# Performance work log

Measured on AMD Instinct MI355X. Metric: run time of the kernel, lower is better.

The kernel has to match this reference:

```python
import jax, jax.numpy as jnp
import numpy as np

H, Wd, Z = 480, 480, 2
BN_EPS = 1e-3  # PointPillars-style BatchNorm1d(eps=1e-3)


def setup_inputs() -> dict:
    key = jax.random.key(0)
    ks = jax.random.split(key, 5)
    bs, seq, N, Cin, C = 2, 1, 20000, 4, 64
    features = jax.random.normal(ks[0], (bs, seq, N, Cin), dtype=jnp.float32)
    cx = jax.random.randint(ks[1], (bs, seq, N), 0, H)
    cy = jax.random.randint(ks[2], (bs, seq, N), 0, Wd)
    cz = jax.random.randint(ks[3], (bs, seq, N), 0, Z)
    coords = jnp.stack([cx, cy, cz], axis=-1).astype(jnp.int64)
    W = jax.random.normal(ks[4], (C, Cin), dtype=jnp.float32) * 0.1
    gamma = jnp.ones((C,), jnp.float32)
    beta = jnp.zeros((C,), jnp.float32)
    running_mean = jnp.zeros((C,), jnp.float32)
    running_var = jnp.ones((C,), jnp.float32)
    return {"features": features, "coords": coords, "W": W, "gamma": gamma,
            "beta": beta, "running_mean": running_mean, "running_var": running_var}


def reference(features, coords, W, gamma, beta, running_mean, running_var):
    bs, seq, N, Cin = features.shape
    feats = features.reshape(bs * seq, N, Cin)          # [B, N, 4]
    co = coords.reshape(bs * seq, N, 3)
    # flattened voxel index: x*W*Z + y*Z + z, in [0, H*W*Z)
    idx = co[:, :, 0] * (Wd * Z) + co[:, :, 1] * Z + co[:, :, 2]  # [B, N]
    # linear (no bias) + BatchNorm1d (inference stats) + ReLU
    x = jnp.einsum('bnc,uc->bnu', feats, W)             # [B, N, 64]
    x = (x - running_mean) * (gamma / jnp.sqrt(running_var + BN_EPS)) + beta
    x = jax.nn.relu(x)
    B, n, c = x.shape
    # scatter-max into a zero-initialized dense grid (matches torch scatter reduce='max' into zeros)
    x_max = jnp.zeros((B, H * Wd * Z, c), x.dtype)
    x_max = x_max.at[jnp.arange(B)[:, None], idx].max(x)  # [B, HWZ, C]
    # [B, HWZ, C] -> [B, C, H, W, Z] -> [B, Z, C, H, W] -> [B, Z*C, H, W]
    x_max = jnp.transpose(x_max, (0, 2, 1)).reshape(B, c, H, Wd, Z)
    x_max = jnp.transpose(x_max, (0, 4, 1, 2, 3)).reshape(B, Z * c, H, Wd)
    x_perm = jnp.transpose(x, (0, 2, 1))                # [B, C, N]
    return x_perm, jnp.squeeze(x_max)
```

## Files before the change

### kernel.cpp

```cpp
#include <hip/hip_runtime.h>

#define HH  480
#define WW  480
#define ZZ  2
#define CC  64
#define CIN 4
#define BN_EPS 1e-3f
#define ROWS  (2 * ZZ * HH)
#define MAXR  256
#define CHALF 32
#define TPAD  484

__global__ __launch_bounds__(256) void pfn_clear_cnt(int* __restrict__ rowcnt)
{
    int i = blockIdx.x * blockDim.x + threadIdx.x;
    if (i < ROWS) rowcnt[i] = 0;
}

__global__ __launch_bounds__(256) void pfn_pass_a(
    const float* __restrict__ feats,
    const int*   __restrict__ coords,
    const float* __restrict__ W,
    const float* __restrict__ gamma,
    const float* __restrict__ beta,
    const float* __restrict__ rmean,
    const float* __restrict__ rvar,
    float*  __restrict__ out0,
    float4* __restrict__ rowf4,
    int*    __restrict__ roww,
    int*    __restrict__ rowcnt,
    int N, int B)
{
    int gid = blockIdx.x * blockDim.x + threadIdx.x;
    int total = B * N;
    if (gid >= total) return;
    int n = gid % N;
    int b = gid / N;

    float4 f = *reinterpret_cast<const float4*>(feats + (long)gid * CIN);

    #pragma unroll 8
    for (int c = 0; c < CC; ++c) {
        float scale = gamma[c] * rsqrtf(rvar[c] + BN_EPS);
        float bias  = beta[c] - rmean[c] * scale;
        float v = f.x * W[c*4+0] + f.y * W[c*4+1] + f.z * W[c*4+2] + f.w * W[c*4+3];
        v = fmaxf(v * scale + bias, 0.0f);
        out0[((long)(b * CC + c)) * N + n] = v;
    }

    int cx = coords[(long)gid*3 + 0];
    int cy = coords[(long)gid*3 + 1];
    int cz = coords[(long)gid*3 + 2];
    int row = (b * ZZ + cz) * HH + cx;
    int k = atomicAdd(&rowcnt[row], 1);
    if (k < MAXR) {
        rowf4[(long)row * MAXR + k] = f;
        roww [(long)row * MAXR + k] = cy;
    }
}

__global__ __launch_bounds__(512) void pfn_pass_b(
    const float4* __restrict__ rowf4,
    const int*    __restrict__ roww,
    const int*    __restrict__ rowcnt,
    const float*  __restrict__ W,
    const float*  __restrict__ gamma,
    const float*  __restrict__ beta,
    const float*  __restrict__ rmean,
    const float*  __restrict__ rvar,
    float* __restrict__ out1)
{
    int bid  = blockIdx.x;
    int half = bid & 1;
    int row  = bid >> 1;
    int h = row % HH;
    int z = (row / HH) % ZZ;
    int b = row / (HH * ZZ);
    const int c0 = half * CHALF;
    const int tid = threadIdx.x;

    __shared__ float tile[CHALF][TPAD];
    __shared__ float lw[4][CHALF], lsc[CHALF], lbi[CHALF];

    float4* t4 = reinterpret_cast<float4*>(&tile[0][0]);
    const int n4z = CHALF * TPAD / 4;
    for (int i = tid; i < n4z; i += 512)
        t4[i] = make_float4(0.f, 0.f, 0.f, 0.f);
    if (tid < CHALF) {
        int c = c0 + tid;
        float s = gamma[c] * rsqrtf(rvar[c] + BN_EPS);
        lsc[tid] = s;
        lbi[tid] = beta[c] - rmean[c] * s;
        lw[0][tid] = W[c*4+0]; lw[1][tid] = W[c*4+1];
        lw[2][tid] = W[c*4+2]; lw[3][tid] = W[c*4+3];
    }
    __syncthreads();

    int cnt = rowcnt[row];
    cnt = cnt < MAXR ? cnt : MAXR;
    const long rb = (long)row * MAXR;

    for (int i = tid; i < cnt * CHALF; i += 512) {
        int j  = i >> 5;
        int cc = i & (CHALF - 1);
        float4 f = rowf4[rb + j];
        int    w = roww [rb + j];
        float v = f.x*lw[0][cc] + f.y*lw[1][cc] + f.z*lw[2][cc] + f.w*lw[3][cc];
        v = fmaxf(v * lsc[cc] + lbi[cc], 0.0f);
        atomicMax(reinterpret_cast<unsigned int*>(&tile[cc][w]), __float_as_uint(v));
    }
    __syncthreads();

    const long plane = (long)HH * WW;
    const long base  = (((long)((b * ZZ + z) * CC + c0)) * HH + h) * WW;
    const int w4row = WW / 4;
    for (int i = tid; i < CHALF * w4row; i += 512) {
        int c  = i / w4row;
        int w4 = i % w4row;
        *reinterpret_cast<float4*>(out1 + base + (long)c * plane + (long)w4 * 4)
            = *reinterpret_cast<const float4*>(&tile[c][w4 * 4]);
    }
}

__global__ __launch_bounds__(256) void pfn_fallback(
    const float* __restrict__ feats, const int* __restrict__ coords,
    const float* __restrict__ W, const float* __restrict__ gamma,
    const float* __restrict__ beta, const float* __restrict__ rmean,
    const float* __restrict__ rvar, float* __restrict__ out0,
    float* __restrict__ out1, int N, int B)
{
    long gid = (long)blockIdx.x * blockDim.x + threadIdx.x;
    long total = (long)CC * B * N;
    if (gid >= total) return;
    int n = (int)(gid % N); int rem = (int)(gid / N);
    int b = rem % B; int c = rem / B;
    long pt = (long)b * N + n;
    float4 f = *reinterpret_cast<const float4*>(feats + pt * CIN);
    float scale = gamma[c] * rsqrtf(rvar[c] + BN_EPS);
    float bias  = beta[c] - rmean[c] * scale;
    float val = f.x*W[c*4] + f.y*W[c*4+1] + f.z*W[c*4+2] + f.w*W[c*4+3];
    val = fmaxf(val * scale + bias, 0.0f);
    out0[((long)(b * CC + c)) * N + n] = val;
    int cx = coords[pt*3+0], cy = coords[pt*3+1], cz = coords[pt*3+2];
    long o1 = ((((long)(b * ZZ + cz)) * CC + c) * HH + cx) * WW + cy;
    atomicMax(reinterpret_cast<unsigned int*>(out1) + o1, __float_as_uint(val));
}

extern "C" void kernel_launch(void* const* d_in, const int* in_sizes, int n_in,
                              void* d_out, int out_size, void* d_ws, size_t ws_size,
                              hipStream_t stream) {
    const float* feats  = (const float*)d_in[0];
    const int*   coords = (const int*)d_in[1];
    const float* W      = (const float*)d_in[2];
    const float* gamma  = (const float*)d_in[3];
    const float* beta   = (const float*)d_in[4];
    const float* rmean  = (const float*)d_in[5];
    const float* rvar   = (const float*)d_in[6];

    const int B = 2;
    const int N = in_sizes[0] / (B * CIN);

    float* out0 = (float*)d_out;
    long   out0_sz = (long)B * CC * N;
    float* out1 = out0 + out0_sz;

    const size_t rowf4_bytes = (size_t)ROWS * MAXR * sizeof(float4);
    const size_t roww_bytes  = (size_t)ROWS * MAXR * sizeof(int);
    const size_t cnt_bytes   = (size_t)ROWS * sizeof(int);
    const size_t need = rowf4_bytes + roww_bytes + cnt_bytes;

    if (ws_size >= need) {
        float4* rowf4  = (float4*)d_ws;
        int*    roww   = (int*)((char*)d_ws + rowf4_bytes);
        int*    rowcnt = (int*)((char*)d_ws + rowf4_bytes + roww_bytes);

        pfn_clear_cnt<<<(ROWS + 255) / 256, 256, 0, stream>>>(rowcnt);

        int totalA = B * N;
        pfn_pass_a<<<(totalA + 255) / 256, 256, 0, stream>>>(
            feats, coords, W, gamma, beta, rmean, rvar, out0,
            rowf4, roww, rowcnt, N, B);

        int blocksB = ROWS * (CC / CHALF);
        pfn_pass_b<<<blocksB, 512, 0, stream>>>(
            rowf4, roww, rowcnt, W, gamma, beta, rmean, rvar, out1);
    } else {
        size_t out1_bytes = (size_t)B * ZZ * CC * HH * WW * sizeof(float);
        (void)hipMemsetAsync(out1, 0, out1_bytes, stream);
        long total = (long)CC * B * N;
        pfn_fallback<<<(int)((total + 255) / 256), 256, 0, stream>>>(
            feats, coords, W, gamma, beta, rmean, rvar, out0, out1, N, B);
    }
}
```

Before: 55.29 us.

## Replace shared-memory atomic tile with per-thread register max over row points

Pass B now assigns each thread one channel and four adjacent columns. Each thread scans all points of the row, staged in shared memory, and accumulates the max in registers before writing a float4 directly. This removes zeroing a large LDS tile, the LDS atomics and the tile readback, and lowers shared-memory use so occupancy can rise. In exchange every thread redundantly evaluates all points in the row, and the grid grows to many small blocks.

```diff
diff --git a/kernel.cpp b/kernel.cpp
--- a/kernel.cpp
+++ b/kernel.cpp
@@ -8,8 +8,7 @@
 #define BN_EPS 1e-3f
 #define ROWS  (2 * ZZ * HH)
 #define MAXR  256
-#define CHALF 32
-#define TPAD  484
+#define CG    4
 
 __global__ __launch_bounds__(256) void pfn_clear_cnt(int* __restrict__ rowcnt)
 {
@@ -70,55 +69,50 @@
     const float*  __restrict__ rvar,
     float* __restrict__ out1)
 {
-    int bid  = blockIdx.x;
-    int half = bid & 1;
-    int row  = bid >> 1;
+    int bid = blockIdx.x;
+    int row = bid % ROWS;
+    int cg  = bid / ROWS;
     int h = row % HH;
     int z = (row / HH) % ZZ;
     int b = row / (HH * ZZ);
-    const int c0 = half * CHALF;
     const int tid = threadIdx.x;
+    const int ci  = tid >> 7;
+    const int w4  = tid & 127;
+    const int c   = cg * CG + ci;
 
-    __shared__ float tile[CHALF][TPAD];
-    __shared__ float lw[4][CHALF], lsc[CHALF], lbi[CHALF];
-
-    float4* t4 = reinterpret_cast<float4*>(&tile[0][0]);
-    const int n4z = CHALF * TPAD / 4;
-    for (int i = tid; i < n4z; i += 512)
-        t4[i] = make_float4(0.f, 0.f, 0.f, 0.f);
-    if (tid < CHALF) {
-        int c = c0 + tid;
-        float s = gamma[c] * rsqrtf(rvar[c] + BN_EPS);
-        lsc[tid] = s;
-        lbi[tid] = beta[c] - rmean[c] * s;
-        lw[0][tid] = W[c*4+0]; lw[1][tid] = W[c*4+1];
-        lw[2][tid] = W[c*4+2]; lw[3][tid] = W[c*4+3];
-    }
-    __syncthreads();
+    __shared__ float4 spt[MAXR];
+    __shared__ int    swd[MAXR];
 
     int cnt = rowcnt[row];
     cnt = cnt < MAXR ? cnt : MAXR;
     const long rb = (long)row * MAXR;
-
-    for (int i = tid; i < cnt * CHALF; i += 512) {
-        int j  = i >> 5;
-        int cc = i & (CHALF - 1);
-        float4 f = rowf4[rb + j];
-        int    w = roww [rb + j];
-        float v = f.x*lw[0][cc] + f.y*lw[1][cc] + f.z*lw[2][cc] + f.w*lw[3][cc];
-        v = fmaxf(v * lsc[cc] + lbi[cc], 0.0f);
-        atomicMax(reinterpret_cast<unsigned int*>(&tile[cc][w]), __float_as_uint(v));
+    for (int j = tid; j < cnt; j += 512) {
+        spt[j] = rowf4[rb + j];
+        swd[j] = roww[rb + j];
     }
     __syncthreads();
 
-    const long plane = (long)HH * WW;
-    const long base  = (((long)((b * ZZ + z) * CC + c0)) * HH + h) * WW;
-    const int w4row = WW / 4;
-    for (int i = tid; i < CHALF * w4row; i += 512) {
-        int c  = i / w4row;
-        int w4 = i % w4row;
-        *reinterpret_cast<float4*>(out1 + base + (long)c * plane + (long)w4 * 4)
-            = *reinterpret_cast<const float4*>(&tile[c][w4 * 4]);
+    const float w0 = W[c*4+0], w1 = W[c*4+1], w2 = W[c*4+2], w3 = W[c*4+3];
+    const float sc = gamma[c] * rsqrtf(rvar[c] + BN_EPS);
+    const float bi = beta[c] - rmean[c] * sc;
+
+    float4 acc = make_float4(0.f, 0.f, 0.f, 0.f);
+    for (int j = 0; j < cnt; ++j) {
+        float4 f = spt[j];
+        int    w = swd[j];
+        float v = f.x*w0 + f.y*w1 + f.z*w2 + f.w*w3;
+        v = fmaxf(v * sc + bi, 0.0f);
+        bool hit = (w >> 2) == w4;
+        int  sl  = w & 3;
+        acc.x = (hit && sl == 0) ? fmaxf(acc.x, v) : acc.x;
+        acc.y = (hit && sl == 1) ? fmaxf(acc.y, v) : acc.y;
+        acc.z = (hit && sl == 2) ? fmaxf(acc.z, v) : acc.z;
+        acc.w = (hit && sl == 3) ? fmaxf(acc.w, v) : acc.w;
+    }
+
+    if (w4 < 120) {
+        long o = (((long)((b * ZZ + z) * CC + c)) * HH + h) * WW + (long)w4 * 4;
+        *reinterpret_cast<float4*>(out1 + o) = acc;
     }
 }
 
@@ -181,7 +175,7 @@
             feats, coords, W, gamma, beta, rmean, rvar, out0,
             rowf4, roww, rowcnt, N, B);
 
-        int blocksB = ROWS * (CC / CHALF);
+        int blocksB = (CC / CG) * ROWS;
         pfn_pass_b<<<blocksB, 512, 0, stream>>>(
             rowf4, roww, rowcnt, W, gamma, beta, rmean, rvar, out1);
     } else {
```

Measured after the change: 202.9 us. 267% more time.
